# Performance work log

Hardware: AMD Instinct MI355X
Metric: run time of the kernel (lower is better)

Reference implementation:

```python
import jax, jax.numpy as jnp
import numpy as np

B, S, D, H = 4, 2048, 128, 8

def setup_inputs() -> dict:
    key = jax.random.key(0)
    ks = jax.random.split(key, 11)
    sc_in = 1.0 / np.sqrt(D)
    sc_out = 1.0 / np.sqrt(H * D)
    return {
        "Q": jax.random.normal(ks[0], (B, S, D), jnp.float32),
        "K": jax.random.normal(ks[1], (B, S, D), jnp.float32),
        "V": jax.random.normal(ks[2], (B, S, D), jnp.float32),
        "WQ_w": jax.random.normal(ks[3], (H * D, D), jnp.float32) * sc_in,
        "WQ_b": jax.random.normal(ks[4], (H * D,), jnp.float32) * 0.01,
        "WK_w": jax.random.normal(ks[5], (H * D, D), jnp.float32) * sc_in,
        "WK_b": jax.random.normal(ks[6], (H * D,), jnp.float32) * 0.01,
        "WV_w": jax.random.normal(ks[7], (H * D, D), jnp.float32) * sc_in,
        "WV_b": jax.random.normal(ks[8], (H * D,), jnp.float32) * 0.01,
        "W_w": jax.random.normal(ks[9], (D, H * D), jnp.float32) * sc_out,
        "W_b": jax.random.normal(ks[10], (D,), jnp.float32) * 0.01,
    }

def reference(Q, K, V, WQ_w, WQ_b, WK_w, WK_b, WV_w, WV_b, W_w, W_b):
    b, s, d = Q.shape
    h = WQ_w.shape[0] // d
    # Linear projections: [b,s,d] -> [b,s,h*d] -> [b,h,s,d]
    rQ = (Q @ WQ_w.T + WQ_b).reshape(b, s, h, d).transpose(0, 2, 1, 3)
    rK = (K @ WK_w.T + WK_b).reshape(b, s, h, d).transpose(0, 2, 1, 3)
    rV = (V @ WV_w.T + WV_b).reshape(b, s, h, d).transpose(0, 2, 1, 3)
    # Scores: [b,h,s,s], scaled by sqrt(head_dim) = sqrt(input_dim)
    scores = jnp.einsum("bhqd,bhkd->bhqk", rQ, rK) / jnp.sqrt(jnp.asarray(d, rQ.dtype))
    sim = jax.nn.softmax(scores, axis=-1)
    # Attend and merge heads: [b,h,s,d] -> [b,s,h*d]
    oV = jnp.einsum("bhqk,bhkd->bqhd", sim, rV).reshape(b, s, h * d)
    return oV @ W_w.T + W_b
```

## Files before the change

### kernel.cpp

```cpp
#include <hip/hip_runtime.h>
#include <hip/hip_bf16.h>

typedef unsigned short u16;
typedef unsigned int   u32;
typedef short v8s __attribute__((ext_vector_type(8)));
typedef float v4f __attribute__((ext_vector_type(4)));
typedef float v16f __attribute__((ext_vector_type(16)));
typedef int   v2i __attribute__((ext_vector_type(2)));

#define MFMA16(a,b,c) __builtin_amdgcn_mfma_f32_16x16x32_bf16(a,b,c,0,0,0)
#define MFMA32(a,b,c) __builtin_amdgcn_mfma_f32_32x32x16_bf16(a,b,c,0,0,0)


__device__ __forceinline__ u16 f2b(float f){ u32 i; __builtin_memcpy(&i,&f,4); u32 r = (i + 0x7FFFu + ((i>>16)&1u))>>16; return (u16)r; }
__device__ __forceinline__ u32 pk2(float a, float b){
  __hip_bfloat162 h = __float22bfloat162_rn(make_float2(a,b));
  u32 r; __builtin_memcpy(&r,&h,4); return r;
}

__device__ __forceinline__ void gl16(const void* g, void* l){
  __builtin_amdgcn_global_load_lds((const __attribute__((address_space(1))) u32*)g,
                                   (__attribute__((address_space(3))) u32*)l, 16, 0, 0);
}

__device__ __forceinline__ void stage8f(const float* g, u16* l){
  float4 a = *(const float4*)g, b = *(const float4*)(g+4);
  uint4 q;
  q.x = pk2(a.x, a.y); q.y = pk2(a.z, a.w);
  q.z = pk2(b.x, b.y); q.w = pk2(b.z, b.w);
  *(uint4*)l = q;
}

__global__ __launch_bounds__(256) void proj_qkv(
    const float* __restrict__ Qx, const float* __restrict__ Kx, const float* __restrict__ Vx,
    const float* __restrict__ WQw, const float* __restrict__ WQb,
    const float* __restrict__ WKw, const float* __restrict__ WKb,
    const float* __restrict__ WVw, const float* __restrict__ WVb,
    u16* __restrict__ Qp, u16* __restrict__ Kp, u16* __restrict__ Vt)
{
  __shared__ u16 smem[32768];
  u16* As = smem;
  u16* Ws = smem + 16384;

  const int z = blockIdx.z;
  const float* X    = (z==0) ? Qx  : (z==1 ? Kx  : Vx);
  const float* W    = (z==0) ? WQw : (z==1 ? WKw : WVw);
  const float* bias = (z==0) ? WQb : (z==1 ? WKb : WVb);
  u16* out          = (z==0) ? Qp  : (z==1 ? Kp  : Vt);
  const float qs    = (z==0) ? 0.12751743076f : 1.0f;

  const int tid = threadIdx.x, wv = tid>>6, lane = tid&63;
  const int quad = lane>>4, l16 = lane&15;
  const int r4 = lane>>2, c4 = lane&3;
  const int m0 = blockIdx.x*128, n0 = blockIdx.y*128;

  for (int idx = wv; idx < 32; idx += 4) {
    int kt = idx >> 3, rg = idx & 7;
    int row = rg*16 + r4;
    stage8f(X + (size_t)(m0+row)*128 + kt*32 + c4*8, &As[kt*4096 + rg*512 + lane*8]);
    stage8f(W + (size_t)(n0+row)*128 + kt*32 + c4*8, &Ws[kt*4096 + rg*512 + lane*8]);
  }
  __syncthreads();

  const int wm = wv & 1, wn = wv >> 1;
  v4f acc[4][4];
#pragma unroll
  for (int i=0;i<4;i++)
#pragma unroll
    for (int j=0;j<4;j++) acc[i][j] = (v4f){0.f,0.f,0.f,0.f};

  if (z < 2) {
#pragma unroll
    for (int ks=0; ks<4; ++ks) {
      v8s af[4], bf[4];
#pragma unroll
      for (int mi=0; mi<4; ++mi) af[mi] = *(const v8s*)&As[ks*4096 + (wm*64+mi*16+l16)*32 + quad*8];
#pragma unroll
      for (int ni=0; ni<4; ++ni) bf[ni] = *(const v8s*)&Ws[ks*4096 + (wn*64+ni*16+l16)*32 + quad*8];
#pragma unroll
      for (int mi=0; mi<4; ++mi)
#pragma unroll
        for (int ni=0; ni<4; ++ni)
          acc[mi][ni] = MFMA16(bf[ni], af[mi], acc[mi][ni]);
    }
#pragma unroll
    for (int ni=0; ni<4; ++ni) {
      int nb = n0 + wn*64 + ni*16 + quad*4;
      float bv0 = bias[nb+0]*qs;
      float bv1 = bias[nb+1]*qs;
      float bv2 = bias[nb+2]*qs;
      float bv3 = bias[nb+3]*qs;
      int h = n0 >> 7, dh = nb & 127;
#pragma unroll
      for (int mi=0; mi<4; ++mi) {
        int m = m0 + wm*64 + mi*16 + l16;
        int b = m >> 11, s = m & 2047;
        uint2 pk;
        pk.x = pk2(fmaf(acc[mi][ni][0], qs, bv0), fmaf(acc[mi][ni][1], qs, bv1));
        pk.y = pk2(fmaf(acc[mi][ni][2], qs, bv2), fmaf(acc[mi][ni][3], qs, bv3));
        *(uint2*)&out[(size_t)(((b<<3) + h)*2048 + s)*128 + dh] = pk;
      }
    }
  } else {
#pragma unroll
    for (int ks=0; ks<4; ++ks) {
      v8s af[4], bf[4];
#pragma unroll
      for (int mi=0; mi<4; ++mi) af[mi] = *(const v8s*)&As[ks*4096 + (wm*64+mi*16+l16)*32 + quad*8];
#pragma unroll
      for (int ni=0; ni<4; ++ni) bf[ni] = *(const v8s*)&Ws[ks*4096 + (wn*64+ni*16+l16)*32 + quad*8];
#pragma unroll
      for (int mi=0; mi<4; ++mi)
#pragma unroll
        for (int ni=0; ni<4; ++ni)
          acc[mi][ni] = MFMA16(af[mi], bf[ni], acc[mi][ni]);
    }
    __syncthreads();
    u16* Cs = smem;
#pragma unroll
    for (int ni=0; ni<4; ++ni) {
      int nl = wn*64 + ni*16 + l16;
      float bv = bias[n0 + nl];
#pragma unroll
      for (int mi=0; mi<4; ++mi) {
        int ml = wm*64 + mi*16 + quad*4;
        uint2 pk;
        pk.x = pk2(acc[mi][ni][0] + bv, acc[mi][ni][1] + bv);
        pk.y = pk2(acc[mi][ni][2] + bv, acc[mi][ni][3] + bv);
        *(uint2*)&Cs[nl*136 + ml] = pk;
      }
    }
    __syncthreads();
    const int nl = tid >> 1;
    const int mb = (tid & 1) * 64;
    const int h = (n0 + nl) >> 7, dh = (n0 + nl) & 127;
    const int b = m0 >> 11, s0 = m0 & 2047;
    size_t gbase = (((size_t)((b<<3) + h)*128 + dh)*2048) + s0 + mb;
    size_t lbase = (size_t)nl*136 + mb;
#pragma unroll
    for (int j = 0; j < 8; ++j)
      *(uint4*)&out[gbase + j*8] = *(const uint4*)&Cs[lbase + j*8];
  }
}

__global__ __launch_bounds__(256, 2) void attn(
    const u16* __restrict__ Qp, const u16* __restrict__ Kp,
    const u16* __restrict__ Vt, u16* __restrict__ O)
{
  __shared__ u16 smem[32768];

  const int tid = threadIdx.x, wv = tid>>6, lane = tid&63;
  const int l32 = lane&31, h = lane>>5;

  const int n  = blockIdx.x;
  const int bh = (n&7)*4 + (n>>7);
  const int q0 = ((n>>3)&15) * 128;

  const u16* Qb = Qp + (size_t)bh*262144 + (size_t)q0*128;
  const u16* Kb = Kp + (size_t)bh*262144;
  const u16* Vb = Vt + (size_t)bh*262144;

  for (int r = 0; r < 8; ++r) {
    int idx = r*256 + tid;
    int kd = idx>>8, q = (idx>>1)&127, hh = idx&1;
    gl16(Qb + q*128 + kd*16 + hh*8, &smem[idx*8]);
  }
  __syncthreads();
  const int qrow = wv*32 + l32;
  v8s qf[8];
#pragma unroll
  for (int kd = 0; kd < 8; ++kd)
    qf[kd] = *(const v8s*)&smem[kd*2048 + qrow*16 + h*8];
  __syncthreads();

  int gK[4], gV[4], lK[4], lV[4];
#pragma unroll
  for (int r = 0; r < 4; ++r) {
    int idx = r*256 + tid;
    lK[r] = idx*8;  lV[r] = 16384 + idx*8;
    int key = idx>>4, pcK = idx&15;
    gK[r] = key*128 + ((pcK ^ (key&15)))*8;
    int d = idx>>3, pcV = idx&7;
    gV[r] = d*2048 + ((pcV ^ (d&7)))*8;
  }
  int kfo[8], vfo[4];
#pragma unroll
  for (int kd = 0; kd < 8; ++kd) kfo[kd] = ((kd*2 + h) ^ (l32 & 15)) * 8;
#pragma unroll
  for (int kt = 0; kt < 4; ++kt) vfo[kt] = ((kt*2 + h) ^ (l32 & 7)) * 8;

  v8s onesf;
#pragma unroll
  for (int j = 0; j < 8; ++j) onesf[j] = (short)0x3F80;

  v16f oacc[4], lacc;
#pragma unroll
  for (int nt = 0; nt < 4; ++nt)
#pragma unroll
    for (int j = 0; j < 16; ++j) oacc[nt][j] = 0.f;
#pragma unroll
  for (int j = 0; j < 16; ++j) lacc[j] = 0.f;

#pragma unroll
  for (int r = 0; r < 4; ++r) gl16(Kb + gK[r], &smem[lK[r]]);
#pragma unroll
  for (int r = 0; r < 4; ++r) gl16(Vb + gV[r], &smem[lV[r]]);

  for (int it = 0; it < 32; ++it) {
    const int cur = it & 1;
    const int ko = cur*8192;
    const int vo = cur*8192;
    __syncthreads();

    if (it + 1 < 32) {
      const u16* Kt  = Kb + (it+1)*8192;
      const u16* Vtt = Vb + (it+1)*64;
      const int po = (cur^1)*8192;
#pragma unroll
      for (int r = 0; r < 4; ++r) gl16(Kt  + gK[r], &smem[po + lK[r]]);
#pragma unroll
      for (int r = 0; r < 4; ++r) gl16(Vtt + gV[r], &smem[po + lV[r] - 16384 + 16384]);
    }

    v16f sa[2];
#pragma unroll
    for (int m = 0; m < 2; ++m)
#pragma unroll
      for (int j = 0; j < 16; ++j) sa[m][j] = 0.f;
    __builtin_amdgcn_s_setprio(1);
#pragma unroll
    for (int kd = 0; kd < 8; ++kd) {
#pragma unroll
      for (int m = 0; m < 2; ++m) {
        v8s kf = *(const v8s*)&smem[ko + (m*32 + l32)*128 + kfo[kd]];
        sa[m] = MFMA32(kf, qf[kd], sa[m]);
      }
    }
    __builtin_amdgcn_s_setprio(0);

    u32 P32[2][4][2];
#pragma unroll
    for (int m = 0; m < 2; ++m)
#pragma unroll
      for (int g = 0; g < 4; ++g) {
        P32[m][g][0] = pk2(__builtin_amdgcn_exp2f(sa[m][g*4+0]),
                           __builtin_amdgcn_exp2f(sa[m][g*4+1]));
        P32[m][g][1] = pk2(__builtin_amdgcn_exp2f(sa[m][g*4+2]),
                           __builtin_amdgcn_exp2f(sa[m][g*4+3]));
      }

    v8s pf[4];
#pragma unroll
    for (int kt = 0; kt < 4; ++kt) {
      const int m = kt >> 1, e = (kt & 1) * 2, o = e + 1;
      union { u32 u[4]; v8s s; } f;
#if __has_builtin(__builtin_amdgcn_permlane32_swap)
      v2i r0 = __builtin_amdgcn_permlane32_swap((int)P32[m][e][0], (int)P32[m][o][0], false, false);
      v2i r1 = __builtin_amdgcn_permlane32_swap((int)P32[m][e][1], (int)P32[m][o][1], false, false);
      f.u[0] = (u32)r0[0]; f.u[1] = (u32)r1[0];
      f.u[2] = (u32)r0[1]; f.u[3] = (u32)r1[1];
#else
      u32 a0 = P32[m][e][0], b0 = P32[m][o][0];
      u32 a1 = P32[m][e][1], b1 = P32[m][o][1];
      asm("v_permlane32_swap_b32 %0, %1" : "+v"(a0), "+v"(b0));
      asm("v_permlane32_swap_b32 %0, %1" : "+v"(a1), "+v"(b1));
      f.u[0] = a0; f.u[1] = a1; f.u[2] = b0; f.u[3] = b1;
#endif
      pf[kt] = f.s;
    }

    __builtin_amdgcn_s_setprio(1);
#pragma unroll
    for (int kt = 0; kt < 4; ++kt) {
      lacc = MFMA32(pf[kt], onesf, lacc);
#pragma unroll
      for (int nt = 0; nt < 4; ++nt) {
        v8s vf = *(const v8s*)&smem[16384 + vo + (nt*32 + l32)*64 + vfo[kt]];
        oacc[nt] = MFMA32(pf[kt], vf, oacc[nt]);
      }
    }
    __builtin_amdgcn_s_setprio(0);
  }

  const int b = bh >> 3, hd = bh & 7;
#pragma unroll
  for (int reg = 0; reg < 16; ++reg) {
    int q = q0 + wv*32 + (reg&3) + 8*(reg>>2) + 4*h;
    float inv = 1.0f / lacc[reg];
    size_t base = ((size_t)(b*2048 + q))*1024 + hd*128;
#pragma unroll
    for (int nt = 0; nt < 4; ++nt)
      O[base + nt*32 + l32] = f2b(oacc[nt][reg] * inv);
  }
}

__global__ __launch_bounds__(256) void outproj(
    const u16* __restrict__ A, const float* __restrict__ Ww,
    const float* __restrict__ Wb, float* __restrict__ out)
{
  __shared__ u16 As[2][2048];
  __shared__ u16 Ws[2][8192];

  const int tid = threadIdx.x, wv = tid>>6, lane = tid&63;
  const int quad = lane>>4, l16 = lane&15;
  const int r4 = lane>>2, c4 = lane&3;
  const int m0 = blockIdx.x*32;

  v4f acc[2][2];
#pragma unroll
  for (int i=0;i<2;i++)
#pragma unroll
    for (int j=0;j<2;j++) acc[i][j] = (v4f){0.f,0.f,0.f,0.f};

  auto stage = [&](int kb, int buf) {
    {
      int kt = wv >> 1, rg = wv & 1;
      int row = rg*16 + r4;
      gl16(A + (size_t)(m0+row)*1024 + kb + kt*32 + c4*8, &As[buf][kt*1024 + rg*512 + lane*8]);
    }
    for (int idx = wv; idx < 16; idx += 4) {
      int kt = idx >> 3, rg = idx & 7;
      int row = rg*16 + r4;
      stage8f(Ww + (size_t)row*1024 + kb + kt*32 + c4*8, &Ws[buf][kt*4096 + rg*512 + lane*8]);
    }
  };

  stage(0, 0);
  for (int kb = 0; kb < 1024; kb += 64) {
    const int cur = (kb >> 6) & 1;
    __syncthreads();
    if (kb + 64 < 1024) stage(kb + 64, cur ^ 1);
#pragma unroll
    for (int ks = 0; ks < 2; ++ks) {
      v8s af0 = *(const v8s*)&As[cur][ks*1024 + (l16)*32 + quad*8];
      v8s af1 = *(const v8s*)&As[cur][ks*1024 + (16 + l16)*32 + quad*8];
#pragma unroll
      for (int nj = 0; nj < 2; ++nj) {
        v8s bf = *(const v8s*)&Ws[cur][ks*4096 + ((wv*2+nj)*16 + l16)*32 + quad*8];
        acc[0][nj] = MFMA16(af0, bf, acc[0][nj]);
        acc[1][nj] = MFMA16(af1, bf, acc[1][nj]);
      }
    }
  }

#pragma unroll
  for (int nj = 0; nj < 2; ++nj) {
    int col = (wv*2+nj)*16 + l16;
    float bv = Wb[col];
#pragma unroll
    for (int mi = 0; mi < 2; ++mi) {
#pragma unroll
      for (int r = 0; r < 4; ++r) {
        int row = m0 + mi*16 + quad*4 + r;
        out[(size_t)row*128 + col] = acc[mi][nj][r] + bv;
      }
    }
  }
}

extern "C" void kernel_launch(void* const* d_in, const int* in_sizes, int n_in,
                              void* d_out, int out_size, void* d_ws, size_t ws_size,
                              hipStream_t stream) {
  const float* Q   = (const float*)d_in[0];
  const float* K   = (const float*)d_in[1];
  const float* V   = (const float*)d_in[2];
  const float* WQw = (const float*)d_in[3];
  const float* WQb = (const float*)d_in[4];
  const float* WKw = (const float*)d_in[5];
  const float* WKb = (const float*)d_in[6];
  const float* WVw = (const float*)d_in[7];
  const float* WVb = (const float*)d_in[8];
  const float* Ww  = (const float*)d_in[9];
  const float* Wb  = (const float*)d_in[10];
  u16* ws = (u16*)d_ws;

  const size_t SZ = (size_t)4*8*2048*128;
  u16* Qp = ws;
  u16* Kp = Qp + SZ;
  u16* Vt = Kp + SZ;
  u16* Ow = Vt + SZ;

  hipLaunchKernelGGL(proj_qkv, dim3(64,8,3), dim3(256), 0, stream,
                     Q,K,V,WQw,WQb,WKw,WKb,WVw,WVb,Qp,Kp,Vt);
  hipLaunchKernelGGL(attn, dim3(512), dim3(256), 0, stream, Qp,Kp,Vt,Ow);
  hipLaunchKernelGGL(outproj, dim3(256), dim3(256), 0, stream, Ow, Ww, Wb, (float*)d_out);
}
```

Measured before the change: 207.6 us.

## Halve attention tile sizes to launch more, smaller workgroups

```diff
diff --git a/kernel.cpp b/kernel.cpp
--- a/kernel.cpp
+++ b/kernel.cpp
@@ -143,26 +143,26 @@
   }
 }
 
-__global__ __launch_bounds__(256, 2) void attn(
+__global__ __launch_bounds__(128, 2) void attn(
     const u16* __restrict__ Qp, const u16* __restrict__ Kp,
     const u16* __restrict__ Vt, u16* __restrict__ O)
 {
-  __shared__ u16 smem[32768];
+  __shared__ u16 smem[16384];
 
   const int tid = threadIdx.x, wv = tid>>6, lane = tid&63;
   const int l32 = lane&31, h = lane>>5;
 
   const int n  = blockIdx.x;
-  const int bh = (n&7)*4 + (n>>7);
-  const int q0 = ((n>>3)&15) * 128;
+  const int bh = (n&7)*4 + (n>>8);
+  const int q0 = ((n>>3)&31) * 64;
 
   const u16* Qb = Qp + (size_t)bh*262144 + (size_t)q0*128;
   const u16* Kb = Kp + (size_t)bh*262144;
   const u16* Vb = Vt + (size_t)bh*262144;
 
   for (int r = 0; r < 8; ++r) {
-    int idx = r*256 + tid;
-    int kd = idx>>8, q = (idx>>1)&127, hh = idx&1;
+    int idx = r*128 + tid;
+    int kd = idx>>7, q = (idx>>1)&63, hh = idx&1;
     gl16(Qb + q*128 + kd*16 + hh*8, &smem[idx*8]);
   }
   __syncthreads();
@@ -170,24 +170,24 @@
   v8s qf[8];
 #pragma unroll
   for (int kd = 0; kd < 8; ++kd)
-    qf[kd] = *(const v8s*)&smem[kd*2048 + qrow*16 + h*8];
+    qf[kd] = *(const v8s*)&smem[kd*1024 + qrow*16 + h*8];
   __syncthreads();
 
   int gK[4], gV[4], lK[4], lV[4];
 #pragma unroll
   for (int r = 0; r < 4; ++r) {
-    int idx = r*256 + tid;
-    lK[r] = idx*8;  lV[r] = 16384 + idx*8;
+    int idx = r*128 + tid;
+    lK[r] = idx*8;  lV[r] = 8192 + idx*8;
     int key = idx>>4, pcK = idx&15;
-    gK[r] = key*128 + ((pcK ^ (key&15)))*8;
-    int d = idx>>3, pcV = idx&7;
-    gV[r] = d*2048 + ((pcV ^ (d&7)))*8;
-  }
-  int kfo[8], vfo[4];
+    gK[r] = key*128 + (pcK ^ (key&15))*8;
+    int d = idx>>2, pcV = idx&3;
+    gV[r] = d*2048 + (pcV ^ ((d>>1)&3))*8;
+  }
+  int kfo[8], vfo[2];
 #pragma unroll
   for (int kd = 0; kd < 8; ++kd) kfo[kd] = ((kd*2 + h) ^ (l32 & 15)) * 8;
 #pragma unroll
-  for (int kt = 0; kt < 4; ++kt) vfo[kt] = ((kt*2 + h) ^ (l32 & 7)) * 8;
+  for (int kt = 0; kt < 2; ++kt) vfo[kt] = ((kt*2 + h) ^ ((l32>>1) & 3)) * 8;
 
   v8s onesf;
 #pragma unroll
@@ -206,62 +206,55 @@
 #pragma unroll
   for (int r = 0; r < 4; ++r) gl16(Vb + gV[r], &smem[lV[r]]);
 
-  for (int it = 0; it < 32; ++it) {
+  for (int it = 0; it < 64; ++it) {
     const int cur = it & 1;
-    const int ko = cur*8192;
-    const int vo = cur*8192;
+    const int ko = cur*4096;
+    const int vo = 8192 + cur*4096;
     __syncthreads();
 
-    if (it + 1 < 32) {
-      const u16* Kt  = Kb + (it+1)*8192;
-      const u16* Vtt = Vb + (it+1)*64;
-      const int po = (cur^1)*8192;
+    if (it + 1 < 64) {
+      const u16* Kt  = Kb + (it+1)*4096;
+      const u16* Vtt = Vb + (it+1)*32;
+      const int po = (cur^1)*4096;
 #pragma unroll
       for (int r = 0; r < 4; ++r) gl16(Kt  + gK[r], &smem[po + lK[r]]);
 #pragma unroll
-      for (int r = 0; r < 4; ++r) gl16(Vtt + gV[r], &smem[po + lV[r] - 16384 + 16384]);
-    }
-
-    v16f sa[2];
-#pragma unroll
-    for (int m = 0; m < 2; ++m)
-#pragma unroll
-      for (int j = 0; j < 16; ++j) sa[m][j] = 0.f;
+      for (int r = 0; r < 4; ++r) gl16(Vtt + gV[r], &smem[po + lV[r]]);
+    }
+
+    v16f sa;
+#pragma unroll
+    for (int j = 0; j < 16; ++j) sa[j] = 0.f;
     __builtin_amdgcn_s_setprio(1);
 #pragma unroll
     for (int kd = 0; kd < 8; ++kd) {
-#pragma unroll
-      for (int m = 0; m < 2; ++m) {
-        v8s kf = *(const v8s*)&smem[ko + (m*32 + l32)*128 + kfo[kd]];
-        sa[m] = MFMA32(kf, qf[kd], sa[m]);
-      }
+      v8s kf = *(const v8s*)&smem[ko + l32*128 + kfo[kd]];
+      sa = MFMA32(kf, qf[kd], sa);
     }
     __builtin_amdgcn_s_setprio(0);
 
-    u32 P32[2][4][2];
-#pragma unroll
-    for (int m = 0; m < 2; ++m)
-#pragma unroll
-      for (int g = 0; g < 4; ++g) {
-        P32[m][g][0] = pk2(__builtin_amdgcn_exp2f(sa[m][g*4+0]),
-                           __builtin_amdgcn_exp2f(sa[m][g*4+1]));
-        P32[m][g][1] = pk2(__builtin_amdgcn_exp2f(sa[m][g*4+2]),
-                           __builtin_amdgcn_exp2f(sa[m][g*4+3]));
-      }
-
-    v8s pf[4];
-#pragma unroll
-    for (int kt = 0; kt < 4; ++kt) {
-      const int m = kt >> 1, e = (kt & 1) * 2, o = e + 1;
+    u32 P32[4][2];
+#pragma unroll
+    for (int g = 0; g < 4; ++g) {
+      P32[g][0] = pk2(__builtin_amdgcn_exp2f(sa[g*4+0]),
+                      __builtin_amdgcn_exp2f(sa[g*4+1]));
+      P32[g][1] = pk2(__builtin_amdgcn_exp2f(sa[g*4+2]),
+                      __builtin_amdgcn_exp2f(sa[g*4+3]));
+    }
+
+    v8s pf[2];
+#pragma unroll
+    for (int kt = 0; kt < 2; ++kt) {
+      const int e = kt*2, o = e + 1;
       union { u32 u[4]; v8s s; } f;
 #if __has_builtin(__builtin_amdgcn_permlane32_swap)
-      v2i r0 = __builtin_amdgcn_permlane32_swap((int)P32[m][e][0], (int)P32[m][o][0], false, false);
-      v2i r1 = __builtin_amdgcn_permlane32_swap((int)P32[m][e][1], (int)P32[m][o][1], false, false);
+      v2i r0 = __builtin_amdgcn_permlane32_swap((int)P32[e][0], (int)P32[o][0], false, false);
+      v2i r1 = __builtin_amdgcn_permlane32_swap((int)P32[e][1], (int)P32[o][1], false, false);
       f.u[0] = (u32)r0[0]; f.u[1] = (u32)r1[0];
       f.u[2] = (u32)r0[1]; f.u[3] = (u32)r1[1];
 #else
-      u32 a0 = P32[m][e][0], b0 = P32[m][o][0];
-      u32 a1 = P32[m][e][1], b1 = P32[m][o][1];
+      u32 a0 = P32[e][0], b0 = P32[o][0];
+      u32 a1 = P32[e][1], b1 = P32[o][1];
       asm("v_permlane32_swap_b32 %0, %1" : "+v"(a0), "+v"(b0));
       asm("v_permlane32_swap_b32 %0, %1" : "+v"(a1), "+v"(b1));
       f.u[0] = a0; f.u[1] = a1; f.u[2] = b0; f.u[3] = b1;
@@ -271,11 +264,11 @@
 
     __builtin_amdgcn_s_setprio(1);
 #pragma unroll
-    for (int kt = 0; kt < 4; ++kt) {
+    for (int kt = 0; kt < 2; ++kt) {
       lacc = MFMA32(pf[kt], onesf, lacc);
 #pragma unroll
       for (int nt = 0; nt < 4; ++nt) {
-        v8s vf = *(const v8s*)&smem[16384 + vo + (nt*32 + l32)*64 + vfo[kt]];
+        v8s vf = *(const v8s*)&smem[vo + (nt*32 + l32)*32 + vfo[kt]];
         oacc[nt] = MFMA32(pf[kt], vf, oacc[nt]);
       }
     }
@@ -382,6 +375,6 @@
 
   hipLaunchKernelGGL(proj_qkv, dim3(64,8,3), dim3(256), 0, stream,
                      Q,K,V,WQw,WQb,WKw,WKb,WVw,WVb,Qp,Kp,Vt);
-  hipLaunchKernelGGL(attn, dim3(512), dim3(256), 0, stream, Qp,Kp,Vt,Ow);
+  hipLaunchKernelGGL(attn, dim3(1024), dim3(128), 0, stream, Qp,Kp,Vt,Ow);
   hipLaunchKernelGGL(outproj, dim3(256), dim3(256), 0, stream, Ow, Ww, Wb, (float*)d_out);
 }
```

New measurement: 223.9 us. 1.08x slower.
